# Performance work log

Hardware: AMD Instinct MI355X
Metric: run time of the kernel (lower is better)

Reference implementation:

```python
import jax, jax.numpy as jnp
import numpy as np

BS, SEQ, NV, DM, K = 128, 2048, 64, 512, 64
MAX_ITER, TOL = 10, 1e-4


def setup_inputs() -> dict:
    key = jax.random.key(0)
    k1, k2, k3, k4 = jax.random.split(key, 4)
    x = jax.random.normal(k1, (BS, SEQ, NV), jnp.float32)
    bound = 1.0 / np.sqrt(SEQ)
    W = jax.random.uniform(k2, (DM, SEQ), jnp.float32, -bound, bound)  # nn.Linear weight
    b = jax.random.uniform(k3, (DM,), jnp.float32, -bound, bound)
    centroids = jax.random.normal(k4, (K, DM), jnp.float32)  # kaiming-uniform-init param (random stand-in)
    return {"x": x, "W": W, "b": b, "centroids": centroids}


def _kmeans(x_emb, centroids):
    # x_emb: [N, DM]; fixed-length scan with a `done` flag emulating torch's tol break.
    N = x_emb.shape[0]
    x_sq = jnp.sum(x_emb * x_emb, axis=1, keepdims=True)  # [N,1]

    def body(state, _):
        cent, ids, done = state
        # squared euclidean distances (argmin-equivalent to cdist p=2)
        d2 = x_sq - 2.0 * (x_emb @ cent.T) + jnp.sum(cent * cent, axis=1)  # [N,K]
        new_ids = jnp.argmin(d2, axis=1)
        sums = jax.ops.segment_sum(x_emb, new_ids, num_segments=K)          # [K,DM]
        counts = jax.ops.segment_sum(jnp.ones((N,), x_emb.dtype), new_ids, num_segments=K)
        means = sums / jnp.maximum(counts, 1.0)[:, None]
        new_cent = jnp.where((counts > 0)[:, None], means, cent)  # empty cluster keeps old centroid
        shift = jnp.linalg.norm(new_cent - cent)
        cent_out = jnp.where(done, cent, new_cent)
        ids_out = jnp.where(done, ids, new_ids)
        done_out = done | (shift < TOL)
        return (cent_out, ids_out, done_out), None

    init = (centroids, jnp.zeros((N,), jnp.int32), jnp.array(False))
    (cent, ids, _), _ = jax.lax.scan(body, init, None, length=MAX_ITER)
    return ids, cent


def reference(x, W, b, centroids):
    # x: [bs, seq, n_vars] -> permute -> linear(seq->d_model) -> [bs*n_vars, d_model]
    xt = jnp.transpose(x, (0, 2, 1))                 # [bs, n_vars, seq]
    x_emb = (xt @ W.T + b).reshape(-1, DM)           # [bs*n_vars, d_model]
    ids, cent = _kmeans(x_emb, centroids)
    prob = jax.nn.one_hot(ids, K, dtype=jnp.float32).reshape(BS, NV, K)
    return prob, cent, x_emb
```

## Files before the change

### kernel.cpp

```cpp
#include <hip/hip_runtime.h>

#define SEQ 2048
#define NVAR 64
#define DMODEL 512
#define BSZ 128
#define KC 64
#define NPT (BSZ*NVAR)
#define MAXIT 10

typedef __bf16 bf16x8 __attribute__((ext_vector_type(8)));
typedef float f32x4 __attribute__((ext_vector_type(4)));

__device__ __forceinline__ void load_lds16(const void* g, void* l) {
  __builtin_amdgcn_global_load_lds((const __attribute__((address_space(1))) void*)g,
                                   (__attribute__((address_space(3))) void*)l, 16, 0, 0);
}

__device__ __forceinline__ unsigned short bf16_rn(float x) {
  unsigned int u = __float_as_uint(x);
  u += 0x7fffu + ((u >> 16) & 1u);
  return (unsigned short)(u >> 16);
}

__global__ __launch_bounds__(256) void init_k(const float* __restrict__ c0,
    float* __restrict__ cent, unsigned short* __restrict__ centh,
    unsigned short* __restrict__ centl, float* __restrict__ cent_sq,
    int* __restrict__ done, float* __restrict__ shift2, int* __restrict__ ticket) {
  const int k = blockIdx.x, t = threadIdx.x;
  __shared__ float red[256];
  float l = 0.f;
  #pragma unroll
  for (int rr = 0; rr < 2; ++rr) {
    int d = t + 256 * rr;
    float v = c0[k * DMODEL + d];
    cent[k * DMODEL + d] = v;
    unsigned short h = bf16_rn(v);
    centh[k * DMODEL + d] = h;
    centl[k * DMODEL + d] = bf16_rn(v - __uint_as_float((unsigned)h << 16));
    l += v * v;
  }
  red[t] = l; __syncthreads();
  for (int s = 128; s > 0; s >>= 1) { if (t < s) red[t] += red[t + s]; __syncthreads(); }
  if (t == 0) cent_sq[k] = red[0];
  if (k == 0 && t < MAXIT) { shift2[t] = 0.f; ticket[t] = 0; }
  if (k == 0 && t == 31) *done = 0;
}

__global__ __launch_bounds__(256) void conv_w(const float* __restrict__ W,
    unsigned short* __restrict__ Wh, unsigned short* __restrict__ Wl) {
  int i = (blockIdx.x * 256 + threadIdx.x) * 4;
  float4 v = *(const float4*)(W + i);
  ushort4 h, l;
  h.x = bf16_rn(v.x); l.x = bf16_rn(v.x - __uint_as_float((unsigned)h.x << 16));
  h.y = bf16_rn(v.y); l.y = bf16_rn(v.y - __uint_as_float((unsigned)h.y << 16));
  h.z = bf16_rn(v.z); l.z = bf16_rn(v.z - __uint_as_float((unsigned)h.z << 16));
  h.w = bf16_rn(v.w); l.w = bf16_rn(v.w - __uint_as_float((unsigned)h.w << 16));
  *(ushort4*)(Wh + i) = h;
  *(ushort4*)(Wl + i) = l;
}

__global__ __launch_bounds__(256) void conv_x(const float* __restrict__ x,
    unsigned short* __restrict__ Xh, unsigned short* __restrict__ Xl) {
  __shared__ float tile[64 * 65];
  const int k0 = blockIdx.x * 64;
  const int bs = blockIdx.y;
  const int t = threadIdx.x;
  const float* xb = x + (size_t)bs * SEQ * NVAR + (size_t)k0 * NVAR;
  #pragma unroll
  for (int p = 0; p < 4; ++p) {
    int idx = t + 256 * p;
    int row = idx >> 4, c4 = (idx & 15) * 4;
    float4 v = *(const float4*)(xb + row * NVAR + c4);
    tile[row * 65 + c4 + 0] = v.x; tile[row * 65 + c4 + 1] = v.y;
    tile[row * 65 + c4 + 2] = v.z; tile[row * 65 + c4 + 3] = v.w;
  }
  __syncthreads();
  const int v = t >> 2;
  const int kc = (t & 3) * 16;
  unsigned short h[16], l[16];
  #pragma unroll
  for (int j = 0; j < 16; ++j) {
    float f = tile[(kc + j) * 65 + v];
    h[j] = bf16_rn(f);
    l[j] = bf16_rn(f - __uint_as_float((unsigned)h[j] << 16));
  }
  size_t off = (size_t)(bs * 64 + v) * SEQ + k0 + kc;
  *(uint4*)(Xh + off)     = *(uint4*)&h[0];
  *(uint4*)(Xh + off + 8) = *(uint4*)&h[8];
  *(uint4*)(Xl + off)     = *(uint4*)&l[0];
  *(uint4*)(Xl + off + 8) = *(uint4*)&l[8];
}

__global__ __launch_bounds__(256) void gemm_mfma(
    const unsigned short* __restrict__ Ah, const unsigned short* __restrict__ Al,
    const unsigned short* __restrict__ Bh, const unsigned short* __restrict__ Bl,
    const float* __restrict__ bias, float* __restrict__ emb) {
  __shared__ unsigned short sAh[64 * 64] __attribute__((aligned(16)));
  __shared__ unsigned short sAl[64 * 64] __attribute__((aligned(16)));
  __shared__ unsigned short sBh[256 * 64] __attribute__((aligned(16)));
  __shared__ unsigned short sBl[256 * 64] __attribute__((aligned(16)));
  const int t = threadIdx.x;
  const int w = t >> 6, lane = t & 63;
  const int m0 = blockIdx.y * 64;
  const int n0 = blockIdx.x * 256;
  const int wn = w * 64;
  const int lrow = lane >> 3, sl8 = lane & 7;
  const int csrc = sl8 ^ lrow;

  f32x4 acc[4][4];
  #pragma unroll
  for (int i = 0; i < 4; ++i)
    #pragma unroll
    for (int j = 0; j < 4; ++j) acc[i][j] = (f32x4){0.f, 0.f, 0.f, 0.f};

  for (int kt = 0; kt < SEQ; kt += 64) {
    __syncthreads();
    #pragma unroll
    for (int i = 0; i < 2; ++i) {
      const int r = w * 16 + i * 8 + lrow;
      const size_t ga = (size_t)(m0 + r) * SEQ + kt + csrc * 8;
      load_lds16(Ah + ga, &sAh[r * 64 + sl8 * 8]);
      load_lds16(Al + ga, &sAl[r * 64 + sl8 * 8]);
    }
    #pragma unroll
    for (int i = 0; i < 8; ++i) {
      const int r = w * 64 + i * 8 + lrow;
      const size_t gb = (size_t)(n0 + r) * SEQ + kt + csrc * 8;
      load_lds16(Bh + gb, &sBh[r * 64 + sl8 * 8]);
      load_lds16(Bl + gb, &sBl[r * 64 + sl8 * 8]);
    }
    __syncthreads();
    #pragma unroll
    for (int kk = 0; kk < 2; ++kk) {
      const int sl = ((kk * 4 + (lane >> 4)) ^ (lane & 7)) * 8;
      bf16x8 ah[4], al[4], bh[4], bl[4];
      #pragma unroll
      for (int mi = 0; mi < 4; ++mi) {
        int off = (mi * 16 + (lane & 15)) * 64 + sl;
        ah[mi] = *(const bf16x8*)&sAh[off];
        al[mi] = *(const bf16x8*)&sAl[off];
      }
      #pragma unroll
      for (int ni = 0; ni < 4; ++ni) {
        int off = (wn + ni * 16 + (lane & 15)) * 64 + sl;
        bh[ni] = *(const bf16x8*)&sBh[off];
        bl[ni] = *(const bf16x8*)&sBl[off];
      }
      #pragma unroll
      for (int mi = 0; mi < 4; ++mi)
        #pragma unroll
        for (int ni = 0; ni < 4; ++ni) {
          acc[mi][ni] = __builtin_amdgcn_mfma_f32_16x16x32_bf16(ah[mi], bh[ni], acc[mi][ni], 0, 0, 0);
          acc[mi][ni] = __builtin_amdgcn_mfma_f32_16x16x32_bf16(ah[mi], bl[ni], acc[mi][ni], 0, 0, 0);
          acc[mi][ni] = __builtin_amdgcn_mfma_f32_16x16x32_bf16(al[mi], bh[ni], acc[mi][ni], 0, 0, 0);
        }
    }
  }
  #pragma unroll
  for (int ni = 0; ni < 4; ++ni) {
    const int n = n0 + wn + ni * 16 + (lane & 15);
    const float bv = bias[n];
    #pragma unroll
    for (int mi = 0; mi < 4; ++mi) {
      const int m = m0 + mi * 16 + (lane >> 4) * 4;
      #pragma unroll
      for (int r = 0; r < 4; ++r)
        emb[(size_t)(m + r) * DMODEL + n] = acc[mi][ni][r] + bv;
    }
  }
}

__global__ __launch_bounds__(256) void gemm_emb(const float* __restrict__ x,
    const float* __restrict__ W, const float* __restrict__ bias,
    float* __restrict__ emb) {
  __shared__ float As[64][64];
  __shared__ float Ws[64][132];
  const int bs = blockIdx.y;
  const int n0 = blockIdx.x * 128;
  const int t = threadIdx.x;
  const int tx = t & 15, ty = t >> 4;
  float bv[8];
  #pragma unroll
  for (int j = 0; j < 8; ++j) bv[j] = bias[n0 + 8 * tx + j];
  float acc[4][8];
  #pragma unroll
  for (int i = 0; i < 4; ++i)
    #pragma unroll
    for (int j = 0; j < 8; ++j) acc[i][j] = 0.f;
  const float* xb = x + (size_t)bs * SEQ * NVAR;
  for (int k0 = 0; k0 < SEQ; k0 += 64) {
    __syncthreads();
    {
      const float4* src = (const float4*)(xb + (size_t)k0 * NVAR);
      float4* dst = (float4*)&As[0][0];
      #pragma unroll
      for (int r = 0; r < 4; ++r) dst[t + 256 * r] = src[t + 256 * r];
    }
    #pragma unroll
    for (int r = 0; r < 8; ++r) {
      int idx = t + 256 * r;
      int k4 = idx & 15, n = idx >> 4;
      float4 wv = *(const float4*)(W + (size_t)(n0 + n) * SEQ + k0 + 4 * k4);
      Ws[4 * k4 + 0][n] = wv.x; Ws[4 * k4 + 1][n] = wv.y;
      Ws[4 * k4 + 2][n] = wv.z; Ws[4 * k4 + 3][n] = wv.w;
    }
    __syncthreads();
    #pragma unroll 8
    for (int kk = 0; kk < 64; ++kk) {
      const float4 a  = *(const float4*)&As[kk][4 * ty];
      const float4 w0 = *(const float4*)&Ws[kk][8 * tx];
      const float4 w1 = *(const float4*)&Ws[kk][8 * tx + 4];
      const float av[4] = {a.x, a.y, a.z, a.w};
      const float wv[8] = {w0.x, w0.y, w0.z, w0.w, w1.x, w1.y, w1.z, w1.w};
      #pragma unroll
      for (int i = 0; i < 4; ++i)
        #pragma unroll
        for (int j = 0; j < 8; ++j)
          acc[i][j] = fmaf(av[i], wv[j], acc[i][j]);
    }
  }
  #pragma unroll
  for (int i = 0; i < 4; ++i) {
    int row = bs * NVAR + 4 * ty + i;
    float4 o0 = make_float4(acc[i][0] + bv[0], acc[i][1] + bv[1],
                            acc[i][2] + bv[2], acc[i][3] + bv[3]);
    float4 o1 = make_float4(acc[i][4] + bv[4], acc[i][5] + bv[5],
                            acc[i][6] + bv[6], acc[i][7] + bv[7]);
    *(float4*)(emb + (size_t)row * DMODEL + n0 + 8 * tx) = o0;
    *(float4*)(emb + (size_t)row * DMODEL + n0 + 8 * tx + 4) = o1;
  }
}

__global__ __launch_bounds__(256) void conv_et(const float* __restrict__ emb,
    unsigned short* __restrict__ Eh, unsigned short* __restrict__ El,
    unsigned short* __restrict__ Eth, unsigned short* __restrict__ Etl) {
  __shared__ unsigned short Lh[64][72];
  __shared__ unsigned short Ll[64][72];
  const int d0 = blockIdx.x * 64;
  const int p0 = blockIdx.y * 64;
  const int t = threadIdx.x;
  #pragma unroll
  for (int q = 0; q < 2; ++q) {
    int idx = t + 256 * q;
    int r = idx >> 3, c = idx & 7;
    const float* src = emb + (size_t)(p0 + r) * DMODEL + d0 + c * 8;
    float4 v0 = *(const float4*)src;
    float4 v1 = *(const float4*)(src + 4);
    unsigned short h[8], l[8];
    const float vv[8] = {v0.x, v0.y, v0.z, v0.w, v1.x, v1.y, v1.z, v1.w};
    #pragma unroll
    for (int j = 0; j < 8; ++j) {
      h[j] = bf16_rn(vv[j]);
      l[j] = bf16_rn(vv[j] - __uint_as_float((unsigned)h[j] << 16));
    }
    size_t eo = (size_t)(p0 + r) * DMODEL + d0 + c * 8;
    *(uint4*)(Eh + eo) = *(uint4*)&h[0];
    *(uint4*)(El + eo) = *(uint4*)&l[0];
    *(uint4*)&Lh[r][c * 8] = *(uint4*)&h[0];
    *(uint4*)&Ll[r][c * 8] = *(uint4*)&l[0];
  }
  __syncthreads();
  #pragma unroll
  for (int q = 0; q < 2; ++q) {
    int idx = t + 256 * q;
    int dd = idx >> 3, pc = idx & 7;
    unsigned short h[8], l[8];
    #pragma unroll
    for (int j = 0; j < 8; ++j) {
      h[j] = Lh[pc * 8 + j][dd];
      l[j] = Ll[pc * 8 + j][dd];
    }
    size_t to = (size_t)(d0 + dd) * NPT + p0 + pc * 8;
    *(uint4*)(Eth + to) = *(uint4*)&h[0];
    *(uint4*)(Etl + to) = *(uint4*)&l[0];
  }
}

__global__ __launch_bounds__(128) void k1_assign(
    const unsigned short* __restrict__ Eh, const unsigned short* __restrict__ El,
    const unsigned short* __restrict__ Ch, const unsigned short* __restrict__ Cl,
    const float* __restrict__ cent_sq, const int* __restrict__ done,
    int* __restrict__ ids, float* __restrict__ pcnt) {
  if (*done) return;
  __shared__ unsigned short sEh[64 * 64] __attribute__((aligned(16)));
  __shared__ unsigned short sEl[64 * 64] __attribute__((aligned(16)));
  __shared__ unsigned short sCh[64 * 64] __attribute__((aligned(16)));
  __shared__ unsigned short sCl[64 * 64] __attribute__((aligned(16)));
  __shared__ float Dmat[64][65];
  __shared__ float csq_l[64];
  __shared__ int cnt_l[64];
  const int t = threadIdx.x;
  const int w = t >> 6, lane = t & 63;
  const int p0 = blockIdx.x * 64;
  const int lrow = lane >> 3, sl8 = lane & 7;
  const int csrc = sl8 ^ lrow;
  if (t < 64) { csq_l[t] = cent_sq[t]; cnt_l[t] = 0; }

  f32x4 acc[2][4];
  #pragma unroll
  for (int i = 0; i < 2; ++i)
    #pragma unroll
    for (int j = 0; j < 4; ++j) acc[i][j] = (f32x4){0.f, 0.f, 0.f, 0.f};

  for (int kt = 0; kt < DMODEL; kt += 64) {
    __syncthreads();
    #pragma unroll
    for (int i = 0; i < 4; ++i) {
      const int r = w * 32 + i * 8 + lrow;
      const size_t ga = (size_t)(p0 + r) * DMODEL + kt + csrc * 8;
      const size_t gc = (size_t)r * DMODEL + kt + csrc * 8;
      load_lds16(Eh + ga, &sEh[r * 64 + sl8 * 8]);
      load_lds16(El + ga, &sEl[r * 64 + sl8 * 8]);
      load_lds16(Ch + gc, &sCh[r * 64 + sl8 * 8]);
      load_lds16(Cl + gc, &sCl[r * 64 + sl8 * 8]);
    }
    __syncthreads();
    #pragma unroll
    for (int kk = 0; kk < 2; ++kk) {
      const int sl = ((kk * 4 + (lane >> 4)) ^ (lane & 7)) * 8;
      bf16x8 eh[2], el[2], ch[4], cl[4];
      #pragma unroll
      for (int mi = 0; mi < 2; ++mi) {
        int off = (w * 32 + mi * 16 + (lane & 15)) * 64 + sl;
        eh[mi] = *(const bf16x8*)&sEh[off];
        el[mi] = *(const bf16x8*)&sEl[off];
      }
      #pragma unroll
      for (int ni = 0; ni < 4; ++ni) {
        int off = (ni * 16 + (lane & 15)) * 64 + sl;
        ch[ni] = *(const bf16x8*)&sCh[off];
        cl[ni] = *(const bf16x8*)&sCl[off];
      }
      #pragma unroll
      for (int mi = 0; mi < 2; ++mi)
        #pragma unroll
        for (int ni = 0; ni < 4; ++ni) {
          acc[mi][ni] = __builtin_amdgcn_mfma_f32_16x16x32_bf16(eh[mi], ch[ni], acc[mi][ni], 0, 0, 0);
          acc[mi][ni] = __builtin_amdgcn_mfma_f32_16x16x32_bf16(eh[mi], cl[ni], acc[mi][ni], 0, 0, 0);
          acc[mi][ni] = __builtin_amdgcn_mfma_f32_16x16x32_bf16(el[mi], ch[ni], acc[mi][ni], 0, 0, 0);
        }
    }
  }
  #pragma unroll
  for (int mi = 0; mi < 2; ++mi)
    #pragma unroll
    for (int ni = 0; ni < 4; ++ni) {
      const int p = w * 32 + mi * 16 + (lane >> 4) * 4;
      const int k = ni * 16 + (lane & 15);
      const float csq = csq_l[k];
      #pragma unroll
      for (int r = 0; r < 4; ++r)
        Dmat[p + r][k] = csq - 2.f * acc[mi][ni][r];
    }
  __syncthreads();
  if (t < 64) {
    float best = Dmat[t][0]; int bi = 0;
    #pragma unroll 8
    for (int k = 1; k < KC; ++k) {
      float v = Dmat[t][k];
      if (v < best) { best = v; bi = k; }
    }
    ids[p0 + t] = bi;
    atomicAdd(&cnt_l[bi], 1);
  }
  __syncthreads();
  if (t < 64) pcnt[blockIdx.x * KC + t] = (float)cnt_l[t];
}

__global__ __launch_bounds__(256) void k2_segsum(
    const unsigned short* __restrict__ Eth, const unsigned short* __restrict__ Etl,
    const int* __restrict__ ids, const int* __restrict__ done,
    float* __restrict__ psum) {
  if (*done) return;
  __shared__ unsigned short sOH[64 * 136] __attribute__((aligned(16)));
  __shared__ unsigned short sTh[128 * 64] __attribute__((aligned(16)));
  __shared__ unsigned short sTl[128 * 64] __attribute__((aligned(16)));
  __shared__ int ids_l[128];
  const int t = threadIdx.x;
  const int w = t >> 6, lane = t & 63;
  const int dq = blockIdx.x, g = blockIdx.y;
  const int lrow = lane >> 3, sl8 = lane & 7;
  const int csrc = sl8 ^ lrow;

  if (t < 128) ids_l[t] = ids[g * 128 + t];
  __syncthreads();
  #pragma unroll
  for (int q = 0; q < 4; ++q) {
    int c = t * 4 + q;
    int cl = c >> 4, pc = c & 15;
    unsigned short v[8];
    #pragma unroll
    for (int j = 0; j < 8; ++j)
      v[j] = (ids_l[pc * 8 + j] == cl) ? (unsigned short)0x3F80 : (unsigned short)0;
    *(uint4*)&sOH[cl * 136 + pc * 8] = *(uint4*)&v[0];
  }

  f32x4 acc[4][2];
  #pragma unroll
  for (int i = 0; i < 4; ++i)
    #pragma unroll
    for (int j = 0; j < 2; ++j) acc[i][j] = (f32x4){0.f, 0.f, 0.f, 0.f};

  for (int kt = 0; kt < 2; ++kt) {
    __syncthreads();
    #pragma unroll
    for (int i = 0; i < 4; ++i) {
      const int rr = w * 32 + i * 8 + lrow;
      const size_t gt = (size_t)(dq * 128 + rr) * NPT + g * 128 + kt * 64 + csrc * 8;
      load_lds16(Eth + gt, &sTh[rr * 64 + sl8 * 8]);
      load_lds16(Etl + gt, &sTl[rr * 64 + sl8 * 8]);
    }
    __syncthreads();
    #pragma unroll
    for (int kk = 0; kk < 2; ++kk) {
      const int quad = lane >> 4;
      const int poff = kt * 64 + kk * 32 + quad * 8;
      bf16x8 a[4], bh[2], bl[2];
      #pragma unroll
      for (int mi = 0; mi < 4; ++mi)
        a[mi] = *(const bf16x8*)&sOH[(mi * 16 + (lane & 15)) * 136 + poff];
      const int sl = ((kk * 4 + quad) ^ (lane & 7)) * 8;
      #pragma unroll
      for (int ni = 0; ni < 2; ++ni) {
        int off = (w * 32 + ni * 16 + (lane & 15)) * 64 + sl;
        bh[ni] = *(const bf16x8*)&sTh[off];
        bl[ni] = *(const bf16x8*)&sTl[off];
      }
      #pragma unroll
      for (int mi = 0; mi < 4; ++mi)
        #pragma unroll
        for (int ni = 0; ni < 2; ++ni) {
          acc[mi][ni] = __builtin_amdgcn_mfma_f32_16x16x32_bf16(a[mi], bh[ni], acc[mi][ni], 0, 0, 0);
          acc[mi][ni] = __builtin_amdgcn_mfma_f32_16x16x32_bf16(a[mi], bl[ni], acc[mi][ni], 0, 0, 0);
        }
    }
  }
  #pragma unroll
  for (int mi = 0; mi < 4; ++mi)
    #pragma unroll
    for (int ni = 0; ni < 2; ++ni) {
      const int cl = mi * 16 + (lane >> 4) * 4;
      const int d = dq * 128 + w * 32 + ni * 16 + (lane & 15);
      #pragma unroll
      for (int r = 0; r < 4; ++r)
        psum[((size_t)g * KC + cl + r) * DMODEL + d] = acc[mi][ni][r];
    }
}

__global__ __launch_bounds__(256) void k3_update(float* __restrict__ cent,
    unsigned short* __restrict__ centh, unsigned short* __restrict__ centl,
    const float* __restrict__ psum, const float* __restrict__ pcnt,
    int* __restrict__ done, float* __restrict__ cent_sq,
    float* __restrict__ shift2, int* __restrict__ ticket, int iter) {
  if (*done) return;
  const int k = blockIdx.x, t = threadIdx.x;
  __shared__ float red[256];
  __shared__ float cnt_s;
  red[t] = (t < 128) ? pcnt[t * KC + k] : 0.f;
  __syncthreads();
  for (int s = 128; s > 0; s >>= 1) { if (t < s) red[t] += red[t + s]; __syncthreads(); }
  if (t == 0) cnt_s = red[0];
  __syncthreads();
  const float count = cnt_s;
  float l_sh = 0.f, l_sq = 0.f;
  #pragma unroll
  for (int rr = 0; rr < 2; ++rr) {
    int d = t + 256 * rr;
    float s = 0.f;
    for (int g = 0; g < 64; ++g)
      s += psum[((size_t)g * KC + k) * DMODEL + d];
    float oldv = cent[k * DMODEL + d];
    float newv = (count > 0.f) ? (s / fmaxf(count, 1.f)) : oldv;
    cent[k * DMODEL + d] = newv;
    unsigned short h = bf16_rn(newv);
    centh[k * DMODEL + d] = h;
    centl[k * DMODEL + d] = bf16_rn(newv - __uint_as_float((unsigned)h << 16));
    float df = newv - oldv;
    l_sh += df * df;
    l_sq += newv * newv;
  }
  red[t] = l_sh; __syncthreads();
  for (int s = 128; s > 0; s >>= 1) { if (t < s) red[t] += red[t + s]; __syncthreads(); }
  float tot_sh = red[0]; __syncthreads();
  red[t] = l_sq; __syncthreads();
  for (int s = 128; s > 0; s >>= 1) { if (t < s) red[t] += red[t + s]; __syncthreads(); }
  if (t == 0) {
    cent_sq[k] = red[0];
    atomicAdd(shift2 + iter, tot_sh);
    __threadfence();
    int tk = atomicAdd(ticket + iter, 1);
    if (tk == 63) {
      float tot = atomicAdd(shift2 + iter, 0.f);
      if (sqrtf(tot) < 1e-4f) *done = 1;
    }
  }
}

__global__ __launch_bounds__(256) void finalize_k(const int* __restrict__ ids,
    const float* __restrict__ cent, float* __restrict__ out) {
  int t = blockIdx.x * 256 + threadIdx.x;
  if (t < NPT * KC) {
    int n = t >> 6, k = t & 63;
    out[t] = (ids[n] == k) ? 1.f : 0.f;
  } else {
    int i = t - NPT * KC;
    if (i < KC * DMODEL) out[NPT * KC + i] = cent[i];
  }
}

extern "C" void kernel_launch(void* const* d_in, const int* in_sizes, int n_in,
                              void* d_out, int out_size, void* d_ws, size_t ws_size,
                              hipStream_t stream) {
  const float* x    = (const float*)d_in[0];
  const float* W    = (const float*)d_in[1];
  const float* bias = (const float*)d_in[2];
  const float* c0   = (const float*)d_in[3];
  float* out = (float*)d_out;
  float* emb_out = out + NPT * KC + KC * DMODEL;

  char* ws = (char*)d_ws;
  unsigned short* Ehi  = (unsigned short*)(ws + 0);
  unsigned short* Elo  = (unsigned short*)(ws + 8388608);
  unsigned short* Eth  = (unsigned short*)(ws + 16777216);
  unsigned short* Etl  = (unsigned short*)(ws + 25165824);
  float* psum    = (float*)(ws + 33554432);
  float* cent    = (float*)(ws + 41943040);
  unsigned short* centh = (unsigned short*)(ws + 42074112);
  unsigned short* centl = (unsigned short*)(ws + 42139648);
  float* cent_sq = (float*)(ws + 42205184);
  float* shift2  = (float*)(ws + 42205440);
  int*   ticket  = (int*)(ws + 42205504);
  int*   done_f  = (int*)(ws + 42205568);
  float* pcnt    = (float*)(ws + 42205632);
  int*   ids     = (int*)(ws + 42238400);
  unsigned short* Xh = (unsigned short*)(ws + 0);
  unsigned short* Xl = (unsigned short*)(ws + 33554432);
  unsigned short* Wh = (unsigned short*)(ws + 67108864);
  unsigned short* Wl = (unsigned short*)(ws + 69206016);
  const size_t need_fast = 71303168;
  (void)n_in; (void)in_sizes; (void)out_size;

  if (ws_size >= need_fast) {
    conv_w<<<1024, 256, 0, stream>>>(W, Wh, Wl);
    conv_x<<<dim3(32, BSZ), 256, 0, stream>>>(x, Xh, Xl);
    gemm_mfma<<<dim3(2, 128), 256, 0, stream>>>(Xh, Xl, Wh, Wl, bias, emb_out);
  } else {
    gemm_emb<<<dim3(4, BSZ), 256, 0, stream>>>(x, W, bias, emb_out);
  }
  init_k<<<KC, 256, 0, stream>>>(c0, cent, centh, centl, cent_sq, done_f, shift2, ticket);
  conv_et<<<dim3(8, 128), 256, 0, stream>>>(emb_out, Ehi, Elo, Eth, Etl);
  for (int it = 0; it < MAXIT; ++it) {
    k1_assign<<<128, 128, 0, stream>>>(Ehi, Elo, centh, centl, cent_sq, done_f, ids, pcnt);
    k2_segsum<<<dim3(4, 64), 256, 0, stream>>>(Eth, Etl, ids, done_f, psum);
    k3_update<<<KC, 256, 0, stream>>>(cent, centh, centl, psum, pcnt, done_f,
                                      cent_sq, shift2, ticket, it);
  }
  finalize_k<<<2176, 256, 0, stream>>>(ids, cent, out);
}
```

Measured before the change: 508.4 us.

## Halve per-block tiles in gemm, assign and update kernels to fill more CUs

Halves the M-tile of the embedding GEMM (grid 256 to 512 blocks) and the point tile of k1_assign (128 to 256 blocks). k3_update is split into four D-quarters per centroid (256 blocks of 128 threads), so centroid squared norms are now stored as four partial sums that k1 adds together. The goal is better occupancy of the 256 CUs on small grids. The cost is less data reuse per block, since each smaller tile reloads the full B/centroid tile, plus a larger ticket count for the convergence check.

```diff
diff --git a/kernel.cpp b/kernel.cpp
--- a/kernel.cpp
+++ b/kernel.cpp
@@ -24,24 +24,36 @@
 
 __global__ __launch_bounds__(256) void init_k(const float* __restrict__ c0,
     float* __restrict__ cent, unsigned short* __restrict__ centh,
-    unsigned short* __restrict__ centl, float* __restrict__ cent_sq,
+    unsigned short* __restrict__ centl, float* __restrict__ csq4,
     int* __restrict__ done, float* __restrict__ shift2, int* __restrict__ ticket) {
   const int k = blockIdx.x, t = threadIdx.x;
   __shared__ float red[256];
-  float l = 0.f;
-  #pragma unroll
-  for (int rr = 0; rr < 2; ++rr) {
-    int d = t + 256 * rr;
-    float v = c0[k * DMODEL + d];
-    cent[k * DMODEL + d] = v;
-    unsigned short h = bf16_rn(v);
+  float v0, v1;
+  {
+    int d = t;
+    v0 = c0[k * DMODEL + d];
+    cent[k * DMODEL + d] = v0;
+    unsigned short h = bf16_rn(v0);
     centh[k * DMODEL + d] = h;
-    centl[k * DMODEL + d] = bf16_rn(v - __uint_as_float((unsigned)h << 16));
-    l += v * v;
-  }
-  red[t] = l; __syncthreads();
-  for (int s = 128; s > 0; s >>= 1) { if (t < s) red[t] += red[t + s]; __syncthreads(); }
-  if (t == 0) cent_sq[k] = red[0];
+    centl[k * DMODEL + d] = bf16_rn(v0 - __uint_as_float((unsigned)h << 16));
+  }
+  {
+    int d = t + 256;
+    v1 = c0[k * DMODEL + d];
+    cent[k * DMODEL + d] = v1;
+    unsigned short h = bf16_rn(v1);
+    centh[k * DMODEL + d] = h;
+    centl[k * DMODEL + d] = bf16_rn(v1 - __uint_as_float((unsigned)h << 16));
+  }
+  red[t] = v0 * v0; __syncthreads();
+  for (int s = 64; s > 0; s >>= 1) { if ((t & 127) < s) red[t] += red[t + s]; __syncthreads(); }
+  if (t == 0)   csq4[0 * KC + k] = red[0];
+  if (t == 128) csq4[1 * KC + k] = red[128];
+  __syncthreads();
+  red[t] = v1 * v1; __syncthreads();
+  for (int s = 64; s > 0; s >>= 1) { if ((t & 127) < s) red[t] += red[t + s]; __syncthreads(); }
+  if (t == 0)   csq4[2 * KC + k] = red[0];
+  if (t == 128) csq4[3 * KC + k] = red[128];
   if (k == 0 && t < MAXIT) { shift2[t] = 0.f; ticket[t] = 0; }
   if (k == 0 && t == 31) *done = 0;
 }
@@ -95,29 +107,28 @@
     const unsigned short* __restrict__ Ah, const unsigned short* __restrict__ Al,
     const unsigned short* __restrict__ Bh, const unsigned short* __restrict__ Bl,
     const float* __restrict__ bias, float* __restrict__ emb) {
-  __shared__ unsigned short sAh[64 * 64] __attribute__((aligned(16)));
-  __shared__ unsigned short sAl[64 * 64] __attribute__((aligned(16)));
+  __shared__ unsigned short sAh[32 * 64] __attribute__((aligned(16)));
+  __shared__ unsigned short sAl[32 * 64] __attribute__((aligned(16)));
   __shared__ unsigned short sBh[256 * 64] __attribute__((aligned(16)));
   __shared__ unsigned short sBl[256 * 64] __attribute__((aligned(16)));
   const int t = threadIdx.x;
   const int w = t >> 6, lane = t & 63;
-  const int m0 = blockIdx.y * 64;
+  const int m0 = blockIdx.y * 32;
   const int n0 = blockIdx.x * 256;
   const int wn = w * 64;
   const int lrow = lane >> 3, sl8 = lane & 7;
   const int csrc = sl8 ^ lrow;
 
-  f32x4 acc[4][4];
-  #pragma unroll
-  for (int i = 0; i < 4; ++i)
+  f32x4 acc[2][4];
+  #pragma unroll
+  for (int i = 0; i < 2; ++i)
     #pragma unroll
     for (int j = 0; j < 4; ++j) acc[i][j] = (f32x4){0.f, 0.f, 0.f, 0.f};
 
   for (int kt = 0; kt < SEQ; kt += 64) {
     __syncthreads();
-    #pragma unroll
-    for (int i = 0; i < 2; ++i) {
-      const int r = w * 16 + i * 8 + lrow;
+    {
+      const int r = w * 8 + lrow;
       const size_t ga = (size_t)(m0 + r) * SEQ + kt + csrc * 8;
       load_lds16(Ah + ga, &sAh[r * 64 + sl8 * 8]);
       load_lds16(Al + ga, &sAl[r * 64 + sl8 * 8]);
@@ -133,9 +144,9 @@
     #pragma unroll
     for (int kk = 0; kk < 2; ++kk) {
       const int sl = ((kk * 4 + (lane >> 4)) ^ (lane & 7)) * 8;
-      bf16x8 ah[4], al[4], bh[4], bl[4];
-      #pragma unroll
-      for (int mi = 0; mi < 4; ++mi) {
+      bf16x8 ah[2], al[2], bh[4], bl[4];
+      #pragma unroll
+      for (int mi = 0; mi < 2; ++mi) {
         int off = (mi * 16 + (lane & 15)) * 64 + sl;
         ah[mi] = *(const bf16x8*)&sAh[off];
         al[mi] = *(const bf16x8*)&sAl[off];
@@ -147,7 +158,7 @@
         bl[ni] = *(const bf16x8*)&sBl[off];
       }
       #pragma unroll
-      for (int mi = 0; mi < 4; ++mi)
+      for (int mi = 0; mi < 2; ++mi)
         #pragma unroll
         for (int ni = 0; ni < 4; ++ni) {
           acc[mi][ni] = __builtin_amdgcn_mfma_f32_16x16x32_bf16(ah[mi], bh[ni], acc[mi][ni], 0, 0, 0);
@@ -161,7 +172,7 @@
     const int n = n0 + wn + ni * 16 + (lane & 15);
     const float bv = bias[n];
     #pragma unroll
-    for (int mi = 0; mi < 4; ++mi) {
+    for (int mi = 0; mi < 2; ++mi) {
       const int m = m0 + mi * 16 + (lane >> 4) * 4;
       #pragma unroll
       for (int r = 0; r < 4; ++r)
@@ -279,38 +290,43 @@
 __global__ __launch_bounds__(128) void k1_assign(
     const unsigned short* __restrict__ Eh, const unsigned short* __restrict__ El,
     const unsigned short* __restrict__ Ch, const unsigned short* __restrict__ Cl,
-    const float* __restrict__ cent_sq, const int* __restrict__ done,
+    const float* __restrict__ csq4, const int* __restrict__ done,
     int* __restrict__ ids, float* __restrict__ pcnt) {
   if (*done) return;
-  __shared__ unsigned short sEh[64 * 64] __attribute__((aligned(16)));
-  __shared__ unsigned short sEl[64 * 64] __attribute__((aligned(16)));
+  __shared__ unsigned short sEh[32 * 64] __attribute__((aligned(16)));
+  __shared__ unsigned short sEl[32 * 64] __attribute__((aligned(16)));
   __shared__ unsigned short sCh[64 * 64] __attribute__((aligned(16)));
   __shared__ unsigned short sCl[64 * 64] __attribute__((aligned(16)));
-  __shared__ float Dmat[64][65];
+  __shared__ float Dmat[32][65];
   __shared__ float csq_l[64];
   __shared__ int cnt_l[64];
   const int t = threadIdx.x;
   const int w = t >> 6, lane = t & 63;
-  const int p0 = blockIdx.x * 64;
+  const int p0 = blockIdx.x * 32;
   const int lrow = lane >> 3, sl8 = lane & 7;
   const int csrc = sl8 ^ lrow;
-  if (t < 64) { csq_l[t] = cent_sq[t]; cnt_l[t] = 0; }
-
-  f32x4 acc[2][4];
-  #pragma unroll
-  for (int i = 0; i < 2; ++i)
-    #pragma unroll
-    for (int j = 0; j < 4; ++j) acc[i][j] = (f32x4){0.f, 0.f, 0.f, 0.f};
+  if (t < 64) {
+    csq_l[t] = csq4[t] + csq4[KC + t] + csq4[2 * KC + t] + csq4[3 * KC + t];
+    cnt_l[t] = 0;
+  }
+
+  f32x4 acc[4];
+  #pragma unroll
+  for (int j = 0; j < 4; ++j) acc[j] = (f32x4){0.f, 0.f, 0.f, 0.f};
 
   for (int kt = 0; kt < DMODEL; kt += 64) {
     __syncthreads();
+    #pragma unroll
+    for (int i = 0; i < 2; ++i) {
+      const int r = w * 16 + i * 8 + lrow;
+      const size_t ga = (size_t)(p0 + r) * DMODEL + kt + csrc * 8;
+      load_lds16(Eh + ga, &sEh[r * 64 + sl8 * 8]);
+      load_lds16(El + ga, &sEl[r * 64 + sl8 * 8]);
+    }
     #pragma unroll
     for (int i = 0; i < 4; ++i) {
       const int r = w * 32 + i * 8 + lrow;
-      const size_t ga = (size_t)(p0 + r) * DMODEL + kt + csrc * 8;
       const size_t gc = (size_t)r * DMODEL + kt + csrc * 8;
-      load_lds16(Eh + ga, &sEh[r * 64 + sl8 * 8]);
-      load_lds16(El + ga, &sEl[r * 64 + sl8 * 8]);
       load_lds16(Ch + gc, &sCh[r * 64 + sl8 * 8]);
       load_lds16(Cl + gc, &sCl[r * 64 + sl8 * 8]);
     }
@@ -318,12 +334,11 @@
     #pragma unroll
     for (int kk = 0; kk < 2; ++kk) {
       const int sl = ((kk * 4 + (lane >> 4)) ^ (lane & 7)) * 8;
-      bf16x8 eh[2], el[2], ch[4], cl[4];
-      #pragma unroll
-      for (int mi = 0; mi < 2; ++mi) {
-        int off = (w * 32 + mi * 16 + (lane & 15)) * 64 + sl;
-        eh[mi] = *(const bf16x8*)&sEh[off];
-        el[mi] = *(const bf16x8*)&sEl[off];
+      bf16x8 eh, el, ch[4], cl[4];
+      {
+        int off = (w * 16 + (lane & 15)) * 64 + sl;
+        eh = *(const bf16x8*)&sEh[off];
+        el = *(const bf16x8*)&sEl[off];
       }
       #pragma unroll
       for (int ni = 0; ni < 4; ++ni) {
@@ -332,28 +347,24 @@
         cl[ni] = *(const bf16x8*)&sCl[off];
       }
       #pragma unroll
-      for (int mi = 0; mi < 2; ++mi)
-        #pragma unroll
-        for (int ni = 0; ni < 4; ++ni) {
-          acc[mi][ni] = __builtin_amdgcn_mfma_f32_16x16x32_bf16(eh[mi], ch[ni], acc[mi][ni], 0, 0, 0);
-          acc[mi][ni] = __builtin_amdgcn_mfma_f32_16x16x32_bf16(eh[mi], cl[ni], acc[mi][ni], 0, 0, 0);
-          acc[mi][ni] = __builtin_amdgcn_mfma_f32_16x16x32_bf16(el[mi], ch[ni], acc[mi][ni], 0, 0, 0);
-        }
-    }
-  }
-  #pragma unroll
-  for (int mi = 0; mi < 2; ++mi)
-    #pragma unroll
-    for (int ni = 0; ni < 4; ++ni) {
-      const int p = w * 32 + mi * 16 + (lane >> 4) * 4;
-      const int k = ni * 16 + (lane & 15);
-      const float csq = csq_l[k];
-      #pragma unroll
-      for (int r = 0; r < 4; ++r)
-        Dmat[p + r][k] = csq - 2.f * acc[mi][ni][r];
-    }
-  __syncthreads();
-  if (t < 64) {
+      for (int ni = 0; ni < 4; ++ni) {
+        acc[ni] = __builtin_amdgcn_mfma_f32_16x16x32_bf16(eh, ch[ni], acc[ni], 0, 0, 0);
+        acc[ni] = __builtin_amdgcn_mfma_f32_16x16x32_bf16(eh, cl[ni], acc[ni], 0, 0, 0);
+        acc[ni] = __builtin_amdgcn_mfma_f32_16x16x32_bf16(el, ch[ni], acc[ni], 0, 0, 0);
+      }
+    }
+  }
+  #pragma unroll
+  for (int ni = 0; ni < 4; ++ni) {
+    const int p = w * 16 + (lane >> 4) * 4;
+    const int k = ni * 16 + (lane & 15);
+    const float csq = csq_l[k];
+    #pragma unroll
+    for (int r = 0; r < 4; ++r)
+      Dmat[p + r][k] = csq - 2.f * acc[ni][r];
+  }
+  __syncthreads();
+  if (t < 32) {
     float best = Dmat[t][0]; int bi = 0;
     #pragma unroll 8
     for (int k = 1; k < KC; ++k) {
@@ -447,49 +458,44 @@
     }
 }
 
-__global__ __launch_bounds__(256) void k3_update(float* __restrict__ cent,
+__global__ __launch_bounds__(128) void k3_update(float* __restrict__ cent,
     unsigned short* __restrict__ centh, unsigned short* __restrict__ centl,
     const float* __restrict__ psum, const float* __restrict__ pcnt,
-    int* __restrict__ done, float* __restrict__ cent_sq,
+    int* __restrict__ done, float* __restrict__ csq4,
     float* __restrict__ shift2, int* __restrict__ ticket, int iter) {
   if (*done) return;
-  const int k = blockIdx.x, t = threadIdx.x;
-  __shared__ float red[256];
+  const int bk = blockIdx.x & 63, dq = blockIdx.x >> 6;
+  const int t = threadIdx.x;
+  __shared__ float red[128];
   __shared__ float cnt_s;
-  red[t] = (t < 128) ? pcnt[t * KC + k] : 0.f;
-  __syncthreads();
-  for (int s = 128; s > 0; s >>= 1) { if (t < s) red[t] += red[t + s]; __syncthreads(); }
+  red[t] = pcnt[(size_t)(2 * t) * KC + bk] + pcnt[(size_t)(2 * t + 1) * KC + bk];
+  __syncthreads();
+  for (int s = 64; s > 0; s >>= 1) { if (t < s) red[t] += red[t + s]; __syncthreads(); }
   if (t == 0) cnt_s = red[0];
   __syncthreads();
   const float count = cnt_s;
-  float l_sh = 0.f, l_sq = 0.f;
-  #pragma unroll
-  for (int rr = 0; rr < 2; ++rr) {
-    int d = t + 256 * rr;
-    float s = 0.f;
-    for (int g = 0; g < 64; ++g)
-      s += psum[((size_t)g * KC + k) * DMODEL + d];
-    float oldv = cent[k * DMODEL + d];
-    float newv = (count > 0.f) ? (s / fmaxf(count, 1.f)) : oldv;
-    cent[k * DMODEL + d] = newv;
-    unsigned short h = bf16_rn(newv);
-    centh[k * DMODEL + d] = h;
-    centl[k * DMODEL + d] = bf16_rn(newv - __uint_as_float((unsigned)h << 16));
-    float df = newv - oldv;
-    l_sh += df * df;
-    l_sq += newv * newv;
-  }
-  red[t] = l_sh; __syncthreads();
-  for (int s = 128; s > 0; s >>= 1) { if (t < s) red[t] += red[t + s]; __syncthreads(); }
+  const int d = dq * 128 + t;
+  float s = 0.f;
+  for (int g = 0; g < 64; ++g)
+    s += psum[((size_t)g * KC + bk) * DMODEL + d];
+  float oldv = cent[bk * DMODEL + d];
+  float newv = (count > 0.f) ? (s / fmaxf(count, 1.f)) : oldv;
+  cent[bk * DMODEL + d] = newv;
+  unsigned short h = bf16_rn(newv);
+  centh[bk * DMODEL + d] = h;
+  centl[bk * DMODEL + d] = bf16_rn(newv - __uint_as_float((unsigned)h << 16));
+  float df = newv - oldv;
+  red[t] = df * df; __syncthreads();
+  for (int s2 = 64; s2 > 0; s2 >>= 1) { if (t < s2) red[t] += red[t + s2]; __syncthreads(); }
   float tot_sh = red[0]; __syncthreads();
-  red[t] = l_sq; __syncthreads();
-  for (int s = 128; s > 0; s >>= 1) { if (t < s) red[t] += red[t + s]; __syncthreads(); }
+  red[t] = newv * newv; __syncthreads();
+  for (int s2 = 64; s2 > 0; s2 >>= 1) { if (t < s2) red[t] += red[t + s2]; __syncthreads(); }
   if (t == 0) {
-    cent_sq[k] = red[0];
+    csq4[dq * KC + bk] = red[0];
     atomicAdd(shift2 + iter, tot_sh);
     __threadfence();
     int tk = atomicAdd(ticket + iter, 1);
-    if (tk == 63) {
+    if (tk == 255) {
       float tot = atomicAdd(shift2 + iter, 0.f);
       if (sqrtf(tot) < 1e-4f) *done = 1;
     }
@@ -527,12 +533,12 @@
   float* cent    = (float*)(ws + 41943040);
   unsigned short* centh = (unsigned short*)(ws + 42074112);
   unsigned short* centl = (unsigned short*)(ws + 42139648);
-  float* cent_sq = (float*)(ws + 42205184);
-  float* shift2  = (float*)(ws + 42205440);
-  int*   ticket  = (int*)(ws + 42205504);
-  int*   done_f  = (int*)(ws + 42205568);
-  float* pcnt    = (float*)(ws + 42205632);
-  int*   ids     = (int*)(ws + 42238400);
+  float* csq4    = (float*)(ws + 42205184);
+  float* shift2  = (float*)(ws + 42206208);
+  int*   ticket  = (int*)(ws + 42206272);
+  int*   done_f  = (int*)(ws + 42206336);
+  float* pcnt    = (float*)(ws + 42206400);
+  int*   ids     = (int*)(ws + 42271936);
   unsigned short* Xh = (unsigned short*)(ws + 0);
   unsigned short* Xl = (unsigned short*)(ws + 33554432);
   unsigned short* Wh = (unsigned short*)(ws + 67108864);
@@ -543,17 +549,17 @@
   if (ws_size >= need_fast) {
     conv_w<<<1024, 256, 0, stream>>>(W, Wh, Wl);
     conv_x<<<dim3(32, BSZ), 256, 0, stream>>>(x, Xh, Xl);
-    gemm_mfma<<<dim3(2, 128), 256, 0, stream>>>(Xh, Xl, Wh, Wl, bias, emb_out);
+    gemm_mfma<<<dim3(2, 256), 256, 0, stream>>>(Xh, Xl, Wh, Wl, bias, emb_out);
   } else {
     gemm_emb<<<dim3(4, BSZ), 256, 0, stream>>>(x, W, bias, emb_out);
   }
-  init_k<<<KC, 256, 0, stream>>>(c0, cent, centh, centl, cent_sq, done_f, shift2, ticket);
+  init_k<<<KC, 256, 0, stream>>>(c0, cent, centh, centl, csq4, done_f, shift2, ticket);
   conv_et<<<dim3(8, 128), 256, 0, stream>>>(emb_out, Ehi, Elo, Eth, Etl);
   for (int it = 0; it < MAXIT; ++it) {
-    k1_assign<<<128, 128, 0, stream>>>(Ehi, Elo, centh, centl, cent_sq, done_f, ids, pcnt);
+    k1_assign<<<256, 128, 0, stream>>>(Ehi, Elo, centh, centl, csq4, done_f, ids, pcnt);
     k2_segsum<<<dim3(4, 64), 256, 0, stream>>>(Eth, Etl, ids, done_f, psum);
-    k3_update<<<KC, 256, 0, stream>>>(cent, centh, centl, psum, pcnt, done_f,
-                                      cent_sq, shift2, ticket, it);
+    k3_update<<<256, 128, 0, stream>>>(cent, centh, centl, psum, pcnt, done_f,
+                                       csq4, shift2, ticket, it);
   }
   finalize_k<<<2176, 256, 0, stream>>>(ids, cent, out);
 }
```

Measured after the change: 477.5 us. 6.1% less time.
